# Performance work log

Hardware: AMD Instinct MI355X
Metric: run time of the kernel (lower is better)

## Reference

```python
import jax, jax.numpy as jnp
import numpy as np

N, E, B = 50000, 800000, 64
D_IN, D_E = 192, 64
NUM_OUT = 256


def setup_inputs() -> dict:
    key = jax.random.key(0)
    ks = jax.random.split(key, 30)
    rn = lambda k, s: jax.random.normal(k, s, dtype=jnp.float32) * 0.05
    return {
        "x": jax.random.normal(ks[0], (N, D_IN), jnp.float32),
        "edge_index": jax.random.randint(ks[1], (2, E), 0, N, dtype=jnp.int32),
        "edge_attr": jax.random.normal(ks[2], (E, D_E), jnp.float32),
        "batch": jnp.sort(jax.random.randint(ks[3], (N,), 0, B, dtype=jnp.int32)),
        "W1": rn(ks[4], (D_IN, 256)), "as1": rn(ks[5], (4, 64)), "ad1": rn(ks[6], (4, 64)),
        "We1": rn(ks[7], (D_E, 256)), "ae1": rn(ks[8], (4, 64)), "b1": rn(ks[9], (256,)),
        "W2": rn(ks[10], (256, 256)), "as2": rn(ks[11], (4, 64)), "ad2": rn(ks[12], (4, 64)),
        "We2": rn(ks[13], (D_E, 256)), "ae2": rn(ks[14], (4, 64)), "b2": rn(ks[15], (256,)),
        "W3": rn(ks[16], (256, 512)), "as3": rn(ks[17], (4, 128)), "ad3": rn(ks[18], (4, 128)),
        "We3": rn(ks[19], (D_E, 512)), "ae3": rn(ks[20], (4, 128)), "b3": rn(ks[21], (128,)),
        "Wa": rn(ks[22], (128, NUM_OUT)), "ba": rn(ks[23], (NUM_OUT,)),
        "Wv": rn(ks[24], (128, 1)), "bv": rn(ks[25], (1,)),
    }


def reference(x, edge_index, edge_attr, batch,
              W1, as1, ad1, We1, ae1, b1,
              W2, as2, ad2, We2, ae2, b2,
              W3, as3, ad3, We3, ae3, b3,
              Wa, ba, Wv, bv):
    Nn = x.shape[0]
    src0, dst0 = edge_index[0], edge_index[1]
    # PyG add_self_loops(fill_value='mean'): self-loop edge_attr = mean of incoming edge_attr
    deg = jax.ops.segment_sum(jnp.ones_like(dst0, dtype=x.dtype), dst0, num_segments=Nn)
    loop_attr = jax.ops.segment_sum(edge_attr, dst0, num_segments=Nn) / jnp.maximum(deg, 1.0)[:, None]
    loop = jnp.arange(Nn, dtype=src0.dtype)
    src = jnp.concatenate([src0, loop])
    dst = jnp.concatenate([dst0, loop])
    ea = jnp.concatenate([edge_attr, loop_attr], axis=0)

    def gat(h, W, a_s, a_d, We, a_e, bias, concat):
        Hh, C = a_s.shape
        hs = (h @ W).reshape(Nn, Hh, C)                       # [N,H,C]
        al_s = (hs * a_s).sum(-1)                             # [N,H]
        al_d = (hs * a_d).sum(-1)                             # [N,H]
        al_e = ((ea @ We).reshape(-1, Hh, C) * a_e).sum(-1)   # [E+N,H]
        alpha = jax.nn.leaky_relu(al_s[src] + al_d[dst] + al_e, 0.2)
        amax = jax.ops.segment_max(alpha, dst, num_segments=Nn)
        w = jnp.exp(alpha - amax[dst])
        denom = jax.ops.segment_sum(w, dst, num_segments=Nn)
        w = w / (denom[dst] + 1e-16)                          # scatter-softmax over dst
        out = jax.ops.segment_sum(hs[src] * w[..., None], dst, num_segments=Nn)
        out = out.reshape(Nn, Hh * C) if concat else out.mean(axis=1)
        return out + bias

    h = jax.nn.relu(gat(x, W1, as1, ad1, We1, ae1, b1, True))
    h = jax.nn.relu(gat(h, W2, as2, ad2, We2, ae2, b2, True))
    h = gat(h, W3, as3, ad3, We3, ae3, b3, False)
    cnt = jax.ops.segment_sum(jnp.ones((Nn,), h.dtype), batch, num_segments=B)
    g = jax.ops.segment_sum(h, batch, num_segments=B) / jnp.maximum(cnt, 1.0)[:, None]
    logits = g @ Wa + ba
    value = g @ Wv + bv
    return jnp.concatenate([logits, value], axis=-1)  # [B, num_outputs+1]
```

## Files before the change

kernel.cpp:

```cpp
#include <hip/hip_runtime.h>
#include <hip/hip_bf16.h>


typedef __attribute__((ext_vector_type(8))) short short8;
typedef __attribute__((ext_vector_type(4))) float floatx4;

#define DEV __device__ __forceinline__

DEV unsigned short f2b(float f) {
  union { float f; unsigned u; } v; v.f = f;
  unsigned r = v.u + 0x7FFFu + ((v.u >> 16) & 1u);
  return (unsigned short)(r >> 16);
}
DEV float b2f(unsigned short u) {
  union { unsigned u; float f; } v; v.u = ((unsigned)u) << 16;
  return v.f;
}

__global__ void k_deg(const int* __restrict__ dst, int* __restrict__ deg, int E) {
  int e = blockIdx.x * 256 + threadIdx.x;
  if (e < E) atomicAdd(&deg[dst[e]], 1);
}

__global__ __launch_bounds__(256) void k_scan1(const int* __restrict__ deg,
    int* __restrict__ rowptr, int* __restrict__ bsum, int N) {
  __shared__ int sd[256];
  int b = blockIdx.x, tid = threadIdx.x;
  int i0 = b * 1024 + tid * 4;
  int v[4]; int s = 0;
#pragma unroll
  for (int j = 0; j < 4; j++) { int i = i0 + j; v[j] = (i < N) ? deg[i] : 0; s += v[j]; }
  sd[tid] = s;
  __syncthreads();
  for (int off = 1; off < 256; off <<= 1) {
    int t = (tid >= off) ? sd[tid - off] : 0;
    __syncthreads();
    sd[tid] += t;
    __syncthreads();
  }
  int run = sd[tid] - s;
#pragma unroll
  for (int j = 0; j < 4; j++) { int i = i0 + j; if (i < N) rowptr[i] = run; run += v[j]; }
  if (tid == 255) bsum[b] = sd[255];
}

__global__ __launch_bounds__(256) void k_scan2(int* __restrict__ bsum, int nb) {
  __shared__ int sd[256];
  int tid = threadIdx.x;
  int v = (tid < nb) ? bsum[tid] : 0;
  sd[tid] = v;
  __syncthreads();
  for (int off = 1; off < 256; off <<= 1) {
    int t = (tid >= off) ? sd[tid - off] : 0;
    __syncthreads();
    sd[tid] += t;
    __syncthreads();
  }
  if (tid < nb) bsum[tid] = sd[tid] - v;
}

__global__ __launch_bounds__(256) void k_scan3(int* __restrict__ rowptr,
    int* __restrict__ cursor, const int* __restrict__ bsum, int N, int E) {
  int b = blockIdx.x, tid = threadIdx.x;
  int add = bsum[b];
  int i0 = b * 1024 + tid * 4;
#pragma unroll
  for (int j = 0; j < 4; j++) {
    int i = i0 + j;
    if (i < N) { int r = rowptr[i] + add; rowptr[i] = r; cursor[i] = r; }
  }
  if (b == 0 && tid == 0) rowptr[N] = E;
}

__global__ void k_scatter(const int* __restrict__ src, const int* __restrict__ dst,
    int* __restrict__ cursor, int2* __restrict__ csr, int E) {
  int e = blockIdx.x * 256 + threadIdx.x;
  if (e < E) {
    int d = dst[e];
    int pos = atomicAdd(&cursor[d], 1);
    csr[pos] = make_int2(src[e], e);
  }
}

__global__ void k_wt(const float* __restrict__ W, unsigned short* __restrict__ Wt,
                     int K, int Nout) {
  int idx = blockIdx.x * 256 + threadIdx.x;
  if (idx < K * Nout) {
    int n = idx / K, k = idx - n * K;
    Wt[idx] = f2b(W[(size_t)k * Nout + n]);
  }
}

__global__ void k_wep(const float* __restrict__ We1, const float* __restrict__ ae1,
                      const float* __restrict__ We2, const float* __restrict__ ae2,
                      const float* __restrict__ We3, const float* __restrict__ ae3,
                      unsigned short* __restrict__ Wept) {
  int t = blockIdx.x * 256 + threadIdx.x;
  int j = t >> 6, c = t & 63;
  int L = j >> 2, h = j & 3;
  const float* We = (L == 0) ? We1 : (L == 1) ? We2 : We3;
  const float* ae = (L == 0) ? ae1 : (L == 1) ? ae2 : ae3;
  int C = (L == 2) ? 128 : 64;
  int HC = 4 * C;
  float s = 0.f;
  for (int cc = 0; cc < C; cc++) s += We[(size_t)c * HC + h * C + cc] * ae[h * C + cc];
  Wept[j * 64 + c] = f2b(s);
  if (t < 256) {
    int jj = 12 + (t >> 6);
    Wept[jj * 64 + (t & 63)] = 0;
  }
}

template<bool A_F32, int OUT_MODE, bool DO_ALD>
__global__ __launch_bounds__(256) void k_gemm(const void* __restrict__ Ap,
    const unsigned short* __restrict__ Bt, void* __restrict__ Cp,
    int M, int Nout, int K, int EN,
    const float* __restrict__ a_s, const float* __restrict__ a_d,
    float* __restrict__ als, float* __restrict__ ald) {
  __shared__ unsigned short As[64][40];
  __shared__ unsigned short Bs[64][40];
  const int tid = threadIdx.x;
  const int wave = tid >> 6, lane = tid & 63;
  const int quad = lane >> 4, l16 = lane & 15;
  const int m0 = blockIdx.x * 64, n0 = blockIdx.y * 64;
  const int arow = tid >> 2, acg = (tid & 3) * 8;
  floatx4 acc[4] = {{0,0,0,0},{0,0,0,0},{0,0,0,0},{0,0,0,0}};
  for (int k0 = 0; k0 < K; k0 += 32) {
    {
      int gm = m0 + arow;
      unsigned short tmp[8];
      if (A_F32) {
        const float* Af = (const float*)Ap;
        if (gm < M) {
          const float4* p = (const float4*)(Af + (size_t)gm * K + k0 + acg);
          float4 u0 = p[0], u1 = p[1];
          tmp[0]=f2b(u0.x); tmp[1]=f2b(u0.y); tmp[2]=f2b(u0.z); tmp[3]=f2b(u0.w);
          tmp[4]=f2b(u1.x); tmp[5]=f2b(u1.y); tmp[6]=f2b(u1.z); tmp[7]=f2b(u1.w);
        } else {
#pragma unroll
          for (int j = 0; j < 8; j++) tmp[j] = 0;
        }
      } else {
        const unsigned short* Ab = (const unsigned short*)Ap;
        uint4 u = {0,0,0,0};
        if (gm < M) u = *(const uint4*)(Ab + (size_t)gm * K + k0 + acg);
        *(uint4*)tmp = u;
      }
      *(uint4*)&As[arow][acg] = *(uint4*)tmp;
      int gn = n0 + arow;
      uint4 bv = {0,0,0,0};
      if (gn < Nout) bv = *(const uint4*)(Bt + (size_t)gn * K + k0 + acg);
      *(uint4*)&Bs[arow][acg] = bv;
    }
    __syncthreads();
    short8 a = *(const short8*)&As[wave * 16 + l16][quad * 8];
#pragma unroll
    for (int t = 0; t < 4; t++) {
      short8 b = *(const short8*)&Bs[t * 16 + l16][quad * 8];
      acc[t] = __builtin_amdgcn_mfma_f32_16x16x32_bf16(a, b, acc[t], 0, 0, 0);
    }
    __syncthreads();
  }
#pragma unroll
  for (int t = 0; t < 4; t++) {
#pragma unroll
    for (int r = 0; r < 4; r++) {
      int row = m0 + wave * 16 + quad * 4 + r;
      int col = n0 + t * 16 + l16;
      float v = acc[t][r];
      if (OUT_MODE == 0) {
        if (row < M && col < Nout)
          ((unsigned short*)Cp)[(size_t)row * Nout + col] = f2b(v);
      } else {
        if (row < M && col < 12)
          ((float*)Cp)[((size_t)(col >> 2) * EN + row) * 4 + (col & 3)] = v;
      }
    }
  }
  if constexpr (DO_ALD) {
    int h = (n0 * 4) / Nout;
#pragma unroll
    for (int r = 0; r < 4; r++) {
      float ps = 0.f, pd = 0.f;
#pragma unroll
      for (int t = 0; t < 4; t++) {
        int col = n0 + t * 16 + l16;
        float v = acc[t][r];
        ps += v * a_s[col];
        pd += v * a_d[col];
      }
#pragma unroll
      for (int off = 1; off < 16; off <<= 1) {
        ps += __shfl_xor(ps, off, 64);
        pd += __shfl_xor(pd, off, 64);
      }
      int row = m0 + wave * 16 + quad * 4 + r;
      if (l16 == 0 && row < M) {
        atomicAdd(&als[row * 4 + h], ps);
        atomicAdd(&ald[row * 4 + h], pd);
      }
    }
  }
}

__global__ void k_loop_ale(const int* __restrict__ rowptr, const int2* __restrict__ csr,
                           float* __restrict__ ale, int N, int E) {
  int n = blockIdx.x * 256 + threadIdx.x;
  if (n >= N) return;
  const size_t EN = (size_t)E + N;
  int s = rowptr[n], e = rowptr[n + 1];
  float a[12];
#pragma unroll
  for (int j = 0; j < 12; j++) a[j] = 0.f;
  for (int p = s; p < e; p++) {
    int eid = csr[p].y;
#pragma unroll
    for (int L = 0; L < 3; L++) {
      float4 v = *(const float4*)(ale + (L * EN + eid) * 4);
      a[L * 4 + 0] += v.x; a[L * 4 + 1] += v.y;
      a[L * 4 + 2] += v.z; a[L * 4 + 3] += v.w;
    }
  }
  float inv = 1.0f / (float)((e - s) > 1 ? (e - s) : 1);
#pragma unroll
  for (int L = 0; L < 3; L++)
    *(float4*)(ale + (L * EN + E + n) * 4) =
        make_float4(a[L*4+0]*inv, a[L*4+1]*inv, a[L*4+2]*inv, a[L*4+3]*inv);
}

template<int VPL, int MODE>
__global__ __launch_bounds__(256) void k_agg(const unsigned short* __restrict__ hs,
    const int* __restrict__ rowptr, const int2* __restrict__ csr,
    const float* __restrict__ ale,
    const float* __restrict__ als, const float* __restrict__ ald,
    const float* __restrict__ bias, unsigned short* __restrict__ outb,
    float* __restrict__ outf, int N, int E) {
  const int HC = 16 * VPL;
  __shared__ float s_w[4][4][16][4];
  __shared__ int   s_s[4][4][16];
  const int wave = threadIdx.x >> 6;
  const int lane = threadIdx.x & 63;
  const int grp  = lane >> 4;
  const int sl   = lane & 15;
  const int hd   = sl >> 2;
  const int node = blockIdx.x * 16 + wave * 4 + grp;
  if (node >= N) return;
  int start = rowptr[node];
  int cnt   = rowptr[node + 1] - start;
  int total = cnt + 1;
  const float4 aldv = *(const float4*)(ald + node * 4);
  float m0=-1e30f, m1=-1e30f, m2=-1e30f, m3=-1e30f;
  float d0=0.f, d1=0.f, d2=0.f, d3=0.f;
  float acc[VPL];
#pragma unroll
  for (int j = 0; j < VPL; j++) acc[j] = 0.f;
  for (int base = 0; base < total; base += 16) {
    int ei = base + sl;
    bool active = ei < total;
    float a0=-1e30f, a1=-1e30f, a2=-1e30f, a3=-1e30f;
    int sidx = node;
    if (active) {
      const float* alep;
      if (ei < cnt) {
        int2 se = csr[start + ei];
        sidx = se.x;
        alep = ale + (size_t)se.y * 4;
      } else {
        alep = ale + ((size_t)E + node) * 4;
      }
      float4 ev = *(const float4*)alep;
      float4 sv = *(const float4*)(als + sidx * 4);
      a0 = sv.x + aldv.x + ev.x;
      a1 = sv.y + aldv.y + ev.y;
      a2 = sv.z + aldv.z + ev.z;
      a3 = sv.w + aldv.w + ev.w;
      a0 = a0 > 0.f ? a0 : 0.2f * a0;
      a1 = a1 > 0.f ? a1 : 0.2f * a1;
      a2 = a2 > 0.f ? a2 : 0.2f * a2;
      a3 = a3 > 0.f ? a3 : 0.2f * a3;
    }
    float c0=a0, c1=a1, c2=a2, c3=a3;
#pragma unroll
    for (int off = 8; off > 0; off >>= 1) {
      c0 = fmaxf(c0, __shfl_xor(c0, off, 64));
      c1 = fmaxf(c1, __shfl_xor(c1, off, 64));
      c2 = fmaxf(c2, __shfl_xor(c2, off, 64));
      c3 = fmaxf(c3, __shfl_xor(c3, off, 64));
    }
    float n0v = fmaxf(m0, c0), n1v = fmaxf(m1, c1), n2v = fmaxf(m2, c2), n3v = fmaxf(m3, c3);
    float p0 = active ? __expf(a0 - n0v) : 0.f;
    float p1 = active ? __expf(a1 - n1v) : 0.f;
    float p2 = active ? __expf(a2 - n2v) : 0.f;
    float p3 = active ? __expf(a3 - n3v) : 0.f;
    float s0=p0, s1=p1, s2=p2, s3=p3;
#pragma unroll
    for (int off = 8; off > 0; off >>= 1) {
      s0 += __shfl_xor(s0, off, 64);
      s1 += __shfl_xor(s1, off, 64);
      s2 += __shfl_xor(s2, off, 64);
      s3 += __shfl_xor(s3, off, 64);
    }
    float r0 = __expf(m0 - n0v), r1 = __expf(m1 - n1v);
    float r2 = __expf(m2 - n2v), r3 = __expf(m3 - n3v);
    d0 = d0 * r0 + s0; d1 = d1 * r1 + s1; d2 = d2 * r2 + s2; d3 = d3 * r3 + s3;
    float rh = hd == 0 ? r0 : hd == 1 ? r1 : hd == 2 ? r2 : r3;
#pragma unroll
    for (int j = 0; j < VPL; j++) acc[j] *= rh;
    m0 = n0v; m1 = n1v; m2 = n2v; m3 = n3v;
    *(float4*)&s_w[wave][grp][sl][0] = make_float4(p0, p1, p2, p3);
    s_s[wave][grp][sl] = sidx;
    __threadfence_block();
    int chunk = total - base; if (chunk > 16) chunk = 16;
    int t = 0;
    for (; t + 2 <= chunk; t += 2) {
      float w0 = s_w[wave][grp][t][hd];     int sp0 = s_s[wave][grp][t];
      float w1 = s_w[wave][grp][t + 1][hd]; int sp1 = s_s[wave][grp][t + 1];
      const unsigned short* r0p = hs + (size_t)sp0 * HC + sl * VPL;
      const unsigned short* r1p = hs + (size_t)sp1 * HC + sl * VPL;
      unsigned short v0[VPL], v1[VPL];
#pragma unroll
      for (int q = 0; q < VPL / 8; q++) ((uint4*)v0)[q] = ((const uint4*)r0p)[q];
#pragma unroll
      for (int q = 0; q < VPL / 8; q++) ((uint4*)v1)[q] = ((const uint4*)r1p)[q];
#pragma unroll
      for (int j = 0; j < VPL; j++) acc[j] += w0 * b2f(v0[j]);
#pragma unroll
      for (int j = 0; j < VPL; j++) acc[j] += w1 * b2f(v1[j]);
    }
    if (t < chunk) {
      float w0 = s_w[wave][grp][t][hd]; int sp0 = s_s[wave][grp][t];
      const unsigned short* r0p = hs + (size_t)sp0 * HC + sl * VPL;
      unsigned short v0[VPL];
#pragma unroll
      for (int q = 0; q < VPL / 8; q++) ((uint4*)v0)[q] = ((const uint4*)r0p)[q];
#pragma unroll
      for (int j = 0; j < VPL; j++) acc[j] += w0 * b2f(v0[j]);
    }
  }
  float dh = hd == 0 ? d0 : hd == 1 ? d1 : hd == 2 ? d2 : d3;
  float inv = 1.0f / (dh + 1e-16f);
  if constexpr (MODE == 0) {
    unsigned short tmp[VPL];
#pragma unroll
    for (int j = 0; j < VPL; j++) {
      float v = acc[j] * inv + bias[sl * VPL + j];
      tmp[j] = f2b(fmaxf(v, 0.f));
    }
    unsigned short* op = outb + (size_t)node * HC + sl * VPL;
#pragma unroll
    for (int q = 0; q < VPL / 8; q++) ((uint4*)op)[q] = ((uint4*)tmp)[q];
  } else {
#pragma unroll
    for (int j = 0; j < VPL; j++) {
      float v = acc[j] * inv;
      v += __shfl_xor(v, 4, 64);
      v += __shfl_xor(v, 8, 64);
      acc[j] = v * 0.25f;
    }
    if (sl < 4) {
      float* op = outf + (size_t)node * (4 * VPL) + sl * VPL;
#pragma unroll
      for (int j = 0; j < VPL; j++) op[j] = acc[j] + bias[sl * VPL + j];
    }
  }
}

__global__ __launch_bounds__(256) void k_pool(const float* __restrict__ out3,
    const int* __restrict__ bat, float* __restrict__ g, int* __restrict__ cntb, int N) {
  int wid = blockIdx.x * 4 + (threadIdx.x >> 6);
  int lane = threadIdx.x & 63;
  int per = (N + 255) / 256;
  int s = wid * per, e = s + per;
  if (e > N) e = N;
  if (s >= e) return;
  int cur = bat[s];
  float ax = 0.f, ay = 0.f; int run = 0;
  for (int n = s; n < e; n++) {
    int b = bat[n];
    if (b != cur) {
      atomicAdd(&g[cur * 128 + lane * 2], ax);
      atomicAdd(&g[cur * 128 + lane * 2 + 1], ay);
      if (lane == 0) atomicAdd(&cntb[cur], run);
      ax = 0.f; ay = 0.f; run = 0; cur = b;
    }
    float2 v = *(const float2*)(out3 + (size_t)n * 128 + lane * 2);
    ax += v.x; ay += v.y; run++;
  }
  atomicAdd(&g[cur * 128 + lane * 2], ax);
  atomicAdd(&g[cur * 128 + lane * 2 + 1], ay);
  if (lane == 0) atomicAdd(&cntb[cur], run);
}

__global__ __launch_bounds__(320) void k_final(const float* __restrict__ g,
    const int* __restrict__ cntb, const float* __restrict__ Wa, const float* __restrict__ ba,
    const float* __restrict__ Wv, const float* __restrict__ bv, float* __restrict__ out) {
  __shared__ float gm[128];
  int b = blockIdx.x, t = threadIdx.x;
  if (t < 128) {
    float c = (float)cntb[b];
    gm[t] = g[b * 128 + t] / fmaxf(c, 1.f);
  }
  __syncthreads();
  if (t < 257) {
    float acc = 0.f;
    if (t < 256) {
      for (int k = 0; k < 128; k++) acc += gm[k] * Wa[k * 256 + t];
      acc += ba[t];
    } else {
      for (int k = 0; k < 128; k++) acc += gm[k] * Wv[k];
      acc += bv[0];
    }
    out[b * 257 + t] = acc;
  }
}

extern "C" void kernel_launch(void* const* d_in, const int* in_sizes, int n_in,
                              void* d_out, int out_size, void* d_ws, size_t ws_size,
                              hipStream_t stream) {
  const float* x   = (const float*)d_in[0];
  const int*   ei  = (const int*)  d_in[1];
  const float* ea  = (const float*)d_in[2];
  const int*   bat = (const int*)  d_in[3];
  const float* W1  = (const float*)d_in[4];
  const float* as1 = (const float*)d_in[5];
  const float* ad1 = (const float*)d_in[6];
  const float* We1 = (const float*)d_in[7];
  const float* ae1 = (const float*)d_in[8];
  const float* b1  = (const float*)d_in[9];
  const float* W2  = (const float*)d_in[10];
  const float* as2 = (const float*)d_in[11];
  const float* ad2 = (const float*)d_in[12];
  const float* We2 = (const float*)d_in[13];
  const float* ae2 = (const float*)d_in[14];
  const float* b2  = (const float*)d_in[15];
  const float* W3  = (const float*)d_in[16];
  const float* as3 = (const float*)d_in[17];
  const float* ad3 = (const float*)d_in[18];
  const float* We3 = (const float*)d_in[19];
  const float* ae3 = (const float*)d_in[20];
  const float* b3  = (const float*)d_in[21];
  const float* Wa  = (const float*)d_in[22];
  const float* ba  = (const float*)d_in[23];
  const float* Wv  = (const float*)d_in[24];
  const float* bv  = (const float*)d_in[25];
  (void)n_in; (void)out_size; (void)ws_size;

  const int N = in_sizes[0] / 192;
  const int E = in_sizes[1] / 2;
  const size_t EN = (size_t)E + N;
  const int* srcv = ei;
  const int* dstv = ei + E;
  const int nb = (N + 1023) / 1024;

  size_t off = 0;
  auto alloc = [&](size_t bytes) -> char* {
    char* p = (char*)d_ws + off;
    off += (bytes + 255) & ~(size_t)255;
    return p;
  };
  int* deg     = (int*)alloc((size_t)N * 4);
  int* rowptr  = (int*)alloc((size_t)(N + 1) * 4);
  int* cursor  = (int*)alloc((size_t)N * 4);
  int* bsum    = (int*)alloc(256 * 4);
  int2* csr    = (int2*)alloc((size_t)E * 8);
  float* ale   = (float*)alloc(3 * EN * 4 * 4);
  unsigned short* Wept = (unsigned short*)alloc(16 * 64 * 2);
  unsigned short* W1t  = (unsigned short*)alloc(256 * 192 * 2);
  unsigned short* W2t  = (unsigned short*)alloc(256 * 256 * 2);
  unsigned short* W3t  = (unsigned short*)alloc(512 * 256 * 2);
  unsigned short* hs   = (unsigned short*)alloc((size_t)N * 512 * 2);
  unsigned short* h1   = (unsigned short*)alloc((size_t)N * 256 * 2);
  unsigned short* h2   = (unsigned short*)alloc((size_t)N * 256 * 2);
  float* out3  = (float*)alloc((size_t)N * 128 * 4);
  float* als_all = (float*)alloc((size_t)N * 4 * 4 * 6);
  float* g     = (float*)alloc(64 * 128 * 4 + 64 * 4);
  int* cntb    = (int*)(g + 64 * 128);
  float* als1 = als_all + (size_t)N * 4 * 0;
  float* ald1 = als_all + (size_t)N * 4 * 1;
  float* als2 = als_all + (size_t)N * 4 * 2;
  float* ald2 = als_all + (size_t)N * 4 * 3;
  float* als3 = als_all + (size_t)N * 4 * 4;
  float* ald3 = als_all + (size_t)N * 4 * 5;

  hipMemsetAsync(deg, 0, (size_t)N * 4, stream);
  hipMemsetAsync(als_all, 0, (size_t)N * 4 * 4 * 6, stream);
  hipMemsetAsync(g, 0, 64 * 128 * 4 + 64 * 4, stream);

  k_deg<<<(E + 255) / 256, 256, 0, stream>>>(dstv, deg, E);
  k_scan1<<<nb, 256, 0, stream>>>(deg, rowptr, bsum, N);
  k_scan2<<<1, 256, 0, stream>>>(bsum, nb);
  k_scan3<<<nb, 256, 0, stream>>>(rowptr, cursor, bsum, N, E);
  k_scatter<<<(E + 255) / 256, 256, 0, stream>>>(srcv, dstv, cursor, csr, E);
  k_wt<<<(192 * 256 + 255) / 256, 256, 0, stream>>>(W1, W1t, 192, 256);
  k_wt<<<(256 * 256 + 255) / 256, 256, 0, stream>>>(W2, W2t, 256, 256);
  k_wt<<<(256 * 512 + 255) / 256, 256, 0, stream>>>(W3, W3t, 256, 512);
  k_wep<<<3, 256, 0, stream>>>(We1, ae1, We2, ae2, We3, ae3, Wept);
  k_gemm<true, 2, false><<<dim3((E + 63) / 64, 1), 256, 0, stream>>>(
      ea, Wept, ale, E, 16, 64, (int)EN, nullptr, nullptr, nullptr, nullptr);
  k_loop_ale<<<(N + 255) / 256, 256, 0, stream>>>(rowptr, csr, ale, N, E);
  k_gemm<true, 0, true><<<dim3((N + 63) / 64, 4), 256, 0, stream>>>(
      x, W1t, hs, N, 256, 192, 0, as1, ad1, als1, ald1);
  k_agg<16, 0><<<(N + 15) / 16, 256, 0, stream>>>(
      hs, rowptr, csr, ale + 0 * EN * 4, als1, ald1, b1, h1, nullptr, N, E);
  k_gemm<false, 0, true><<<dim3((N + 63) / 64, 4), 256, 0, stream>>>(
      h1, W2t, hs, N, 256, 256, 0, as2, ad2, als2, ald2);
  k_agg<16, 0><<<(N + 15) / 16, 256, 0, stream>>>(
      hs, rowptr, csr, ale + 1 * EN * 4, als2, ald2, b2, h2, nullptr, N, E);
  k_gemm<false, 0, true><<<dim3((N + 63) / 64, 8), 256, 0, stream>>>(
      h2, W3t, hs, N, 512, 256, 0, as3, ad3, als3, ald3);
  k_agg<32, 1><<<(N + 15) / 16, 256, 0, stream>>>(
      hs, rowptr, csr, ale + 2 * EN * 4, als3, ald3, b3, nullptr, out3, N, E);
  k_pool<<<64, 256, 0, stream>>>(out3, bat, g, cntb, N);
  k_final<<<64, 320, 0, stream>>>(g, cntb, Wa, ba, Wv, bv, (float*)d_out);
}
```

Measured before the change: 1.064 ms.

## Drop online softmax max in GAT aggregation and batch neighbor gathers per lane

```diff
diff --git a/kernel.cpp b/kernel.cpp
--- a/kernel.cpp
+++ b/kernel.cpp
@@ -229,116 +229,69 @@
 }
 
 template<int VPL, int MODE>
-__global__ __launch_bounds__(256) void k_agg(const unsigned short* __restrict__ hs,
+__global__ __launch_bounds__(256) void k_gath(const unsigned short* __restrict__ hs,
     const int* __restrict__ rowptr, const int2* __restrict__ csr,
     const float* __restrict__ ale,
     const float* __restrict__ als, const float* __restrict__ ald,
     const float* __restrict__ bias, unsigned short* __restrict__ outb,
     float* __restrict__ outf, int N, int E) {
+  constexpr int U = (VPL == 16) ? 8 : 4;
+  constexpr int NV = VPL / 8;
   const int HC = 16 * VPL;
-  __shared__ float s_w[4][4][16][4];
-  __shared__ int   s_s[4][4][16];
-  const int wave = threadIdx.x >> 6;
   const int lane = threadIdx.x & 63;
-  const int grp  = lane >> 4;
-  const int sl   = lane & 15;
-  const int hd   = sl >> 2;
-  const int node = blockIdx.x * 16 + wave * 4 + grp;
+  const int grp = lane >> 4, sl = lane & 15, hd = sl >> 2;
+  const int node = blockIdx.x * 16 + (threadIdx.x >> 6) * 4 + grp;
   if (node >= N) return;
-  int start = rowptr[node];
-  int cnt   = rowptr[node + 1] - start;
-  int total = cnt + 1;
-  const float4 aldv = *(const float4*)(ald + node * 4);
-  float m0=-1e30f, m1=-1e30f, m2=-1e30f, m3=-1e30f;
-  float d0=0.f, d1=0.f, d2=0.f, d3=0.f;
+  const int start = rowptr[node];
+  const int cnt = rowptr[node + 1] - start;
+  const float aldh = ald[node * 4 + hd];
   float acc[VPL];
 #pragma unroll
   for (int j = 0; j < VPL; j++) acc[j] = 0.f;
-  for (int base = 0; base < total; base += 16) {
-    int ei = base + sl;
-    bool active = ei < total;
-    float a0=-1e30f, a1=-1e30f, a2=-1e30f, a3=-1e30f;
-    int sidx = node;
-    if (active) {
-      const float* alep;
-      if (ei < cnt) {
-        int2 se = csr[start + ei];
-        sidx = se.x;
-        alep = ale + (size_t)se.y * 4;
-      } else {
-        alep = ale + ((size_t)E + node) * 4;
-      }
-      float4 ev = *(const float4*)alep;
-      float4 sv = *(const float4*)(als + sidx * 4);
-      a0 = sv.x + aldv.x + ev.x;
-      a1 = sv.y + aldv.y + ev.y;
-      a2 = sv.z + aldv.z + ev.z;
-      a3 = sv.w + aldv.w + ev.w;
-      a0 = a0 > 0.f ? a0 : 0.2f * a0;
-      a1 = a1 > 0.f ? a1 : 0.2f * a1;
-      a2 = a2 > 0.f ? a2 : 0.2f * a2;
-      a3 = a3 > 0.f ? a3 : 0.2f * a3;
-    }
-    float c0=a0, c1=a1, c2=a2, c3=a3;
-#pragma unroll
-    for (int off = 8; off > 0; off >>= 1) {
-      c0 = fmaxf(c0, __shfl_xor(c0, off, 64));
-      c1 = fmaxf(c1, __shfl_xor(c1, off, 64));
-      c2 = fmaxf(c2, __shfl_xor(c2, off, 64));
-      c3 = fmaxf(c3, __shfl_xor(c3, off, 64));
-    }
-    float n0v = fmaxf(m0, c0), n1v = fmaxf(m1, c1), n2v = fmaxf(m2, c2), n3v = fmaxf(m3, c3);
-    float p0 = active ? __expf(a0 - n0v) : 0.f;
-    float p1 = active ? __expf(a1 - n1v) : 0.f;
-    float p2 = active ? __expf(a2 - n2v) : 0.f;
-    float p3 = active ? __expf(a3 - n3v) : 0.f;
-    float s0=p0, s1=p1, s2=p2, s3=p3;
-#pragma unroll
-    for (int off = 8; off > 0; off >>= 1) {
-      s0 += __shfl_xor(s0, off, 64);
-      s1 += __shfl_xor(s1, off, 64);
-      s2 += __shfl_xor(s2, off, 64);
-      s3 += __shfl_xor(s3, off, 64);
-    }
-    float r0 = __expf(m0 - n0v), r1 = __expf(m1 - n1v);
-    float r2 = __expf(m2 - n2v), r3 = __expf(m3 - n3v);
-    d0 = d0 * r0 + s0; d1 = d1 * r1 + s1; d2 = d2 * r2 + s2; d3 = d3 * r3 + s3;
-    float rh = hd == 0 ? r0 : hd == 1 ? r1 : hd == 2 ? r2 : r3;
-#pragma unroll
-    for (int j = 0; j < VPL; j++) acc[j] *= rh;
-    m0 = n0v; m1 = n1v; m2 = n2v; m3 = n3v;
-    *(float4*)&s_w[wave][grp][sl][0] = make_float4(p0, p1, p2, p3);
-    s_s[wave][grp][sl] = sidx;
-    __threadfence_block();
-    int chunk = total - base; if (chunk > 16) chunk = 16;
-    int t = 0;
-    for (; t + 2 <= chunk; t += 2) {
-      float w0 = s_w[wave][grp][t][hd];     int sp0 = s_s[wave][grp][t];
-      float w1 = s_w[wave][grp][t + 1][hd]; int sp1 = s_s[wave][grp][t + 1];
-      const unsigned short* r0p = hs + (size_t)sp0 * HC + sl * VPL;
-      const unsigned short* r1p = hs + (size_t)sp1 * HC + sl * VPL;
-      unsigned short v0[VPL], v1[VPL];
-#pragma unroll
-      for (int q = 0; q < VPL / 8; q++) ((uint4*)v0)[q] = ((const uint4*)r0p)[q];
-#pragma unroll
-      for (int q = 0; q < VPL / 8; q++) ((uint4*)v1)[q] = ((const uint4*)r1p)[q];
-#pragma unroll
-      for (int j = 0; j < VPL; j++) acc[j] += w0 * b2f(v0[j]);
-#pragma unroll
-      for (int j = 0; j < VPL; j++) acc[j] += w1 * b2f(v1[j]);
-    }
-    if (t < chunk) {
-      float w0 = s_w[wave][grp][t][hd]; int sp0 = s_s[wave][grp][t];
-      const unsigned short* r0p = hs + (size_t)sp0 * HC + sl * VPL;
-      unsigned short v0[VPL];
-#pragma unroll
-      for (int q = 0; q < VPL / 8; q++) ((uint4*)v0)[q] = ((const uint4*)r0p)[q];
-#pragma unroll
-      for (int j = 0; j < VPL; j++) acc[j] += w0 * b2f(v0[j]);
-    }
-  }
-  float dh = hd == 0 ? d0 : hd == 1 ? d1 : hd == 2 ? d2 : d3;
-  float inv = 1.0f / (dh + 1e-16f);
+  float den = 0.f;
+  for (int base = 0; base < cnt; base += U) {
+    int sp[U]; float pw[U];
+#pragma unroll
+    for (int e = 0; e < U; e++) {
+      int idx = base + e;
+      int idc = idx < cnt ? idx : cnt - 1;
+      int2 se = csr[start + idc];
+      sp[e] = se.x;
+      float av = als[(size_t)se.x * 4 + hd] + aldh + ale[(size_t)se.y * 4 + hd];
+      av = av > 0.f ? av : 0.2f * av;
+      float p = __expf(av);
+      pw[e] = idx < cnt ? p : 0.f;
+    }
+    uint4 dv[U][NV];
+#pragma unroll
+    for (int e = 0; e < U; e++) {
+      const uint4* rp = (const uint4*)(hs + (size_t)sp[e] * HC + sl * VPL);
+#pragma unroll
+      for (int q = 0; q < NV; q++) dv[e][q] = rp[q];
+    }
+#pragma unroll
+    for (int e = 0; e < U; e++) {
+      den += pw[e];
+      const unsigned short* vs = (const unsigned short*)&dv[e][0];
+#pragma unroll
+      for (int j = 0; j < VPL; j++) acc[j] += pw[e] * b2f(vs[j]);
+    }
+  }
+  {
+    float av = als[(size_t)node * 4 + hd] + aldh + ale[((size_t)E + node) * 4 + hd];
+    av = av > 0.f ? av : 0.2f * av;
+    float p = __expf(av);
+    den += p;
+    const uint4* rp = (const uint4*)(hs + (size_t)node * HC + sl * VPL);
+#pragma unroll
+    for (int q = 0; q < NV; q++) {
+      uint4 u = rp[q];
+      const unsigned short* vs = (const unsigned short*)&u;
+#pragma unroll
+      for (int j = 0; j < 8; j++) acc[q * 8 + j] += p * b2f(vs[j]);
+    }
+  }
+  float inv = 1.0f / (den + 1e-16f);
   if constexpr (MODE == 0) {
     unsigned short tmp[VPL];
 #pragma unroll
@@ -348,7 +301,7 @@
     }
     unsigned short* op = outb + (size_t)node * HC + sl * VPL;
 #pragma unroll
-    for (int q = 0; q < VPL / 8; q++) ((uint4*)op)[q] = ((uint4*)tmp)[q];
+    for (int q = 0; q < NV; q++) ((uint4*)op)[q] = ((uint4*)tmp)[q];
   } else {
 #pragma unroll
     for (int j = 0; j < VPL; j++) {
@@ -500,15 +453,15 @@
   k_loop_ale<<<(N + 255) / 256, 256, 0, stream>>>(rowptr, csr, ale, N, E);
   k_gemm<true, 0, true><<<dim3((N + 63) / 64, 4), 256, 0, stream>>>(
       x, W1t, hs, N, 256, 192, 0, as1, ad1, als1, ald1);
-  k_agg<16, 0><<<(N + 15) / 16, 256, 0, stream>>>(
+  k_gath<16, 0><<<(N + 15) / 16, 256, 0, stream>>>(
       hs, rowptr, csr, ale + 0 * EN * 4, als1, ald1, b1, h1, nullptr, N, E);
   k_gemm<false, 0, true><<<dim3((N + 63) / 64, 4), 256, 0, stream>>>(
       h1, W2t, hs, N, 256, 256, 0, as2, ad2, als2, ald2);
-  k_agg<16, 0><<<(N + 15) / 16, 256, 0, stream>>>(
+  k_gath<16, 0><<<(N + 15) / 16, 256, 0, stream>>>(
       hs, rowptr, csr, ale + 1 * EN * 4, als2, ald2, b2, h2, nullptr, N, E);
   k_gemm<false, 0, true><<<dim3((N + 63) / 64, 8), 256, 0, stream>>>(
       h2, W3t, hs, N, 512, 256, 0, as3, ad3, als3, ald3);
-  k_agg<32, 1><<<(N + 15) / 16, 256, 0, stream>>>(
+  k_gath<32, 1><<<(N + 15) / 16, 256, 0, stream>>>(
       hs, rowptr, csr, ale + 2 * EN * 4, als3, ald3, b3, nullptr, out3, N, E);
   k_pool<<<64, 256, 0, stream>>>(out3, bat, g, cntb, N);
   k_final<<<64, 320, 0, stream>>>(g, cntb, Wa, ba, Wv, bv, (float*)d_out);
```

New measurement: 1.148 ms. +7.9%, slower.
